# Performance work log

Hardware: AMD Instinct MI355X
Metric: run time of the kernel (lower is better)

## Reference

```python
import jax, jax.numpy as jnp
import numpy as np

N_HEAD = 16
ROPE_THETA = 10000.0


def setup_inputs() -> dict:
    key = jax.random.key(0)
    k0, k1, k2 = jax.random.split(key, 3)
    B, T, C = 2, 2048, 1024
    s = 0.02  # GPT-2 style init scale
    return {
        "x": jax.random.normal(k0, (B, T, C), jnp.float32),
        "w_attn": jax.random.normal(k1, (C, 3 * C), jnp.float32) * s,
        "b_attn": jnp.zeros((3 * C,), jnp.float32),
        "w_proj": jax.random.normal(k2, (C, C), jnp.float32) * s,
        "b_proj": jnp.zeros((C,), jnp.float32),
    }


def _rope(x):
    # x: [B, H, T, D]; interleaved-pair rotary (lucidrains rotate_queries_or_keys)
    T, D = x.shape[-2], x.shape[-1]
    inv_freq = 1.0 / (ROPE_THETA ** (jnp.arange(0, D, 2, dtype=jnp.float32) / D))
    freqs = jnp.arange(T, dtype=jnp.float32)[:, None] * inv_freq[None, :]  # [T, D/2]
    emb = jnp.repeat(freqs, 2, axis=-1)  # [T, D], each freq duplicated per pair
    cos, sin = jnp.cos(emb), jnp.sin(emb)
    xr = x.reshape(*x.shape[:-1], D // 2, 2)
    x1, x2 = xr[..., 0], xr[..., 1]
    rot = jnp.stack((-x2, x1), axis=-1).reshape(x.shape)  # rotate_half
    return x * cos + rot * sin


def reference(x, w_attn, b_attn, w_proj, b_proj):
    B, T, C = x.shape
    H = N_HEAD
    D = C // H
    qkv = x @ w_attn + b_attn                      # [B, T, 3C]
    q, k, v = jnp.split(qkv, 3, axis=-1)

    def heads(t):
        return t.reshape(B, T, H, D).transpose(0, 2, 1, 3)  # [B, H, T, D]

    q, k, v = heads(q), heads(k), heads(v)
    q = _rope(q)
    k = _rope(k)

    att = jnp.einsum("bhqd,bhkd->bhqk", q, k) * (1.0 / np.sqrt(D))
    causal = jnp.tril(jnp.ones((T, T), dtype=bool))
    att = jnp.where(causal, att, -jnp.inf)
    att = jax.nn.softmax(att, axis=-1)
    y = jnp.einsum("bhqk,bhkd->bhqd", att, v)
    y = y.transpose(0, 2, 1, 3).reshape(B, T, C)
    return y @ w_proj + b_proj
```

## Files before the change

### kernel.cpp

```cpp
#include <hip/hip_runtime.h>
#include <hip/hip_bf16.h>
#include <stdint.h>

typedef __hip_bfloat16 bf16;
typedef __attribute__((ext_vector_type(8))) short bf16x8;
typedef __attribute__((ext_vector_type(4))) short bf16x4;
typedef __attribute__((ext_vector_type(4))) float f32x4;

__device__ inline float bf2f(bf16 v) { return __bfloat162float(v); }
__device__ inline bf16 f2bf(float f) { return __float2bfloat16(f); }

__device__ inline void glds16(const void* g, void* l) {
    __builtin_amdgcn_global_load_lds(
        (const __attribute__((address_space(1))) uint32_t*)g,
        (__attribute__((address_space(3))) uint32_t*)l, 16, 0, 0);
}

__device__ inline void conv_wt_tile(const float* __restrict__ W,
                                    bf16* __restrict__ Wt, int N, int K,
                                    int bx, int by, int tid, bf16 (*t)[72])
{
    const int n0 = bx * 64, k0 = by * 64;
#pragma unroll
    for (int p = 0; p < 4; ++p) {
        int idx = p * 256 + tid;
        int kr = idx >> 4, c4 = idx & 15;
        float4 f = *(const float4*)(W + (size_t)(k0 + kr) * N + n0 + c4 * 4);
        t[kr][c4 * 4 + 0] = f2bf(f.x); t[kr][c4 * 4 + 1] = f2bf(f.y);
        t[kr][c4 * 4 + 2] = f2bf(f.z); t[kr][c4 * 4 + 3] = f2bf(f.w);
    }
    __syncthreads();
#pragma unroll
    for (int p = 0; p < 2; ++p) {
        int idx = p * 256 + tid;
        int nr = idx >> 3, ch = idx & 7;
        union { bf16x8 v; bf16 e[8]; } u;
#pragma unroll
        for (int j = 0; j < 8; ++j) u.e[j] = t[ch * 8 + j][nr];
        *(bf16x8*)(Wt + (size_t)(n0 + nr) * K + k0 + ch * 8) = u.v;
    }
}

__global__ __launch_bounds__(256) void prep(
    const float* __restrict__ x, bf16* __restrict__ xbf,
    const float* __restrict__ w_attn, bf16* __restrict__ wat,
    const float* __restrict__ w_proj, bf16* __restrict__ wpt,
    float2* __restrict__ tab)
{
    __shared__ bf16 t[64][72];
    const int bid = blockIdx.x;
    const int tid = threadIdx.x;
    if (bid < 2048) {
        size_t i = ((size_t)bid * 256 + tid) * 8;
        float4 f0 = *(const float4*)(x + i);
        float4 f1 = *(const float4*)(x + i + 4);
        union { bf16x8 v; bf16 e[8]; } u;
        u.e[0] = f2bf(f0.x); u.e[1] = f2bf(f0.y); u.e[2] = f2bf(f0.z); u.e[3] = f2bf(f0.w);
        u.e[4] = f2bf(f1.x); u.e[5] = f2bf(f1.y); u.e[6] = f2bf(f1.z); u.e[7] = f2bf(f1.w);
        *(bf16x8*)(xbf + i) = u.v;
    } else if (bid < 2816) {
        int idx = bid - 2048;
        conv_wt_tile(w_attn, wat, 3072, 1024, idx % 48, idx / 48, tid, t);
    } else if (bid < 3072) {
        int idx = bid - 2816;
        conv_wt_tile(w_proj, wpt, 1024, 1024, idx % 16, idx / 16, tid, t);
    } else {
        int gid = (bid - 3072) * 256 + tid;
        int p = gid & 31, tt = gid >> 5;
        float invf = expf(-(float)(2 * p) * (9.210340371976184f / 64.0f));
        float sn, cs;
        sincosf((float)tt * invf, &sn, &cs);
        tab[gid] = make_float2(cs, sn);
    }
}

__global__ __launch_bounds__(256) void gemm_qkv(
    const bf16* __restrict__ A, const bf16* __restrict__ Bt,
    const float* __restrict__ bias, const float2* __restrict__ tab,
    bf16* __restrict__ qh, bf16* __restrict__ kh, bf16* __restrict__ vt)
{
    const int K = 1024;
    __shared__ __align__(16) bf16 sa[128 * 64];
    __shared__ __align__(16) bf16 sb[128 * 64];

    const int tid  = threadIdx.x;
    const int wave = tid >> 6, lane = tid & 63;
    const int quad = lane >> 4, l16 = lane & 15;
    const int wm = wave >> 1, wn = wave & 1;
    const int row0 = blockIdx.x * 128, n0 = blockIdx.y * 128;

    f32x4 acc[4][4] = {};

    const int srow = lane >> 3;
    const int schk = lane & 7;

    for (int k0 = 0; k0 < K; k0 += 64) {
        __syncthreads();
#pragma unroll
        for (int half = 0; half < 2; ++half) {
#pragma unroll
            for (int g = 0; g < 2; ++g) {
                int rowb = half * 64 + wave * 16 + g * 8;
                int row  = rowb + srow;
                glds16(A + (size_t)(row0 + row) * K + k0 + ((schk ^ row) & 7) * 8,
                       &sa[rowb * 64]);
                glds16(Bt + (size_t)(n0 + row) * K + k0 + ((schk ^ row) & 7) * 8,
                       &sb[rowb * 64]);
            }
        }
        __syncthreads();

#pragma unroll
        for (int kk = 0; kk < 2; ++kk) {
            bf16x8 af[4], bfr[4];
#pragma unroll
            for (int mi = 0; mi < 4; ++mi) {
                int row = wm * 64 + mi * 16 + l16;
                af[mi] = *(const bf16x8*)&sa[row * 64 + (((kk * 4 + quad) ^ row) & 7) * 8];
            }
#pragma unroll
            for (int ni = 0; ni < 4; ++ni) {
                int row = wn * 64 + ni * 16 + l16;
                bfr[ni] = *(const bf16x8*)&sb[row * 64 + (((kk * 4 + quad) ^ row) & 7) * 8];
            }
#pragma unroll
            for (int mi = 0; mi < 4; ++mi)
#pragma unroll
                for (int ni = 0; ni < 4; ++ni)
                    acc[mi][ni] = __builtin_amdgcn_mfma_f32_16x16x32_bf16(
                        af[mi], bfr[ni], acc[mi][ni], 0, 0, 0);
        }
    }

    const float QS = 0.125f * 1.44269504088896f;
#pragma unroll
    for (int ni = 0; ni < 4; ++ni) {
        int col = n0 + wn * 64 + ni * 16 + l16;
        float bvv = bias[col];
        int sec = col >> 10;
        int cd  = col & 1023;
        int h   = cd >> 6, d = cd & 63;
        if (sec == 2) {
#pragma unroll
            for (int mi = 0; mi < 4; ++mi) {
                int trow = row0 + wm * 64 + mi * 16 + quad * 4;
                int tt0 = trow & 2047, bb = trow >> 11;
                union { bf16x4 v; bf16 e[4]; } pv;
#pragma unroll
                for (int r = 0; r < 4; ++r) pv.e[r] = f2bf(acc[mi][ni][r] + bvv);
                *(bf16x4*)(vt + ((size_t)((bb * 16 + h) * 64 + d)) * 2048 + tt0) = pv.v;
            }
        } else {
            int p   = d >> 1;
            bool odd = (d & 1) != 0;
#pragma unroll
            for (int mi = 0; mi < 4; ++mi) {
#pragma unroll
                for (int r = 0; r < 4; ++r) {
                    int row = row0 + wm * 64 + mi * 16 + quad * 4 + r;
                    float v = acc[mi][ni][r] + bvv;
                    float vp = __shfl_xor(v, 1);
                    int tt = row & 2047, b = row >> 11;
                    float2 cssn = tab[tt * 32 + p];
                    float ro = odd ? (v * cssn.x + vp * cssn.y)
                                   : (v * cssn.x - vp * cssn.y);
                    size_t dst = (((size_t)(b * 16 + h)) * 2048 + tt) * 64 + d;
                    if (sec == 0) qh[dst] = f2bf(ro * QS);
                    else          kh[dst] = f2bf(ro);
                }
            }
        }
    }
}

__global__ __launch_bounds__(256) void gemm_proj(
    const bf16* __restrict__ A, const bf16* __restrict__ Bt,
    const float* __restrict__ bias, float* __restrict__ out)
{
    const int N = 1024, K = 1024;
    __shared__ __align__(16) bf16 sa[64 * 64];
    __shared__ __align__(16) bf16 sb[128 * 64];

    const int tid  = threadIdx.x;
    const int wave = tid >> 6, lane = tid & 63;
    const int quad = lane >> 4, l16 = lane & 15;
    const int row0 = blockIdx.x * 64, n0 = blockIdx.y * 128;

    f32x4 acc[4][2] = {};

    const int srow = lane >> 3;
    const int schk = lane & 7;

    for (int k0 = 0; k0 < K; k0 += 64) {
        __syncthreads();
#pragma unroll
        for (int g = 0; g < 2; ++g) {
            int rowb = wave * 16 + g * 8;
            int row  = rowb + srow;
            glds16(A + (size_t)(row0 + row) * K + k0 + ((schk ^ row) & 7) * 8,
                   &sa[rowb * 64]);
        }
#pragma unroll
        for (int g = 0; g < 4; ++g) {
            int rowb = wave * 32 + g * 8;
            int row  = rowb + srow;
            glds16(Bt + (size_t)(n0 + row) * K + k0 + ((schk ^ row) & 7) * 8,
                   &sb[rowb * 64]);
        }
        __syncthreads();

#pragma unroll
        for (int kk = 0; kk < 2; ++kk) {
            bf16x8 af[4], bfr[2];
#pragma unroll
            for (int mi = 0; mi < 4; ++mi) {
                int row = mi * 16 + l16;
                af[mi] = *(const bf16x8*)&sa[row * 64 + (((kk * 4 + quad) ^ row) & 7) * 8];
            }
#pragma unroll
            for (int ni = 0; ni < 2; ++ni) {
                int row = wave * 32 + ni * 16 + l16;
                bfr[ni] = *(const bf16x8*)&sb[row * 64 + (((kk * 4 + quad) ^ row) & 7) * 8];
            }
#pragma unroll
            for (int mi = 0; mi < 4; ++mi)
#pragma unroll
                for (int ni = 0; ni < 2; ++ni)
                    acc[mi][ni] = __builtin_amdgcn_mfma_f32_16x16x32_bf16(
                        af[mi], bfr[ni], acc[mi][ni], 0, 0, 0);
        }
    }

#pragma unroll
    for (int ni = 0; ni < 2; ++ni) {
        int col = n0 + wave * 32 + ni * 16 + l16;
        float bvv = bias[col];
#pragma unroll
        for (int mi = 0; mi < 4; ++mi) {
#pragma unroll
            for (int r = 0; r < 4; ++r) {
                int row = row0 + mi * 16 + quad * 4 + r;
                out[(size_t)row * N + col] = acc[mi][ni][r] + bvv;
            }
        }
    }
}

__global__ __launch_bounds__(256) void attn_k(
    const bf16* __restrict__ qg, const bf16* __restrict__ kg,
    const bf16* __restrict__ vtg, bf16* __restrict__ y)
{
    __shared__ __align__(16) bf16 sK[128 * 64];
    __shared__ __align__(16) bf16 sV[64 * 128];
    __shared__ __align__(16) bf16 pL[4][16][136];

    const int tid  = threadIdx.x;
    const int wave = tid >> 6, lane = tid & 63;
    const int quad = lane >> 4, l16 = lane & 15;
    const int bh   = blockIdx.x;
    const int qt   = 31 - (int)blockIdx.y;
    const bf16* Q  = qg  + (size_t)bh * 2048 * 64;
    const bf16* K  = kg  + (size_t)bh * 2048 * 64;
    const bf16* Vt = vtg + (size_t)bh * 64 * 2048;
    const int b = bh >> 4, h = bh & 15;

    const int q0 = qt * 64 + wave * 16;

    bf16x8 aq[2];
    aq[0] = *(const bf16x8*)(Q + (size_t)(q0 + l16) * 64 + quad * 8);
    aq[1] = *(const bf16x8*)(Q + (size_t)(q0 + l16) * 64 + 32 + quad * 8);

    union { bf16x8 v; short e[8]; } uo;
#pragma unroll
    for (int j = 0; j < 8; ++j) uo.e[j] = (short)0x3F80;
    const bf16x8 vones = uo.v;

    f32x4 o[4] = {};
    f32x4 ls   = {};
    float m_r[4] = {-1e30f, -1e30f, -1e30f, -1e30f};
    const float THR = 8.0f;

    for (int kt = 0; kt <= q0 + 15; kt += 128) {
        __syncthreads();
#pragma unroll
        for (int c = 0; c < 4; ++c) {
            int key = wave * 32 + c * 8 + (lane >> 3);
            int p = lane & 7;
            glds16(K + (size_t)(kt + key) * 64 + ((p ^ key) & 7) * 8,
                   &sK[(wave * 32 + c * 8) * 64]);
        }
#pragma unroll
        for (int c = 0; c < 4; ++c) {
            int d = wave * 16 + c * 4 + (lane >> 4);
            int p = lane & 15;
            glds16(Vt + (size_t)d * 2048 + kt + ((p ^ d) & 15) * 8,
                   &sV[(wave * 16 + c * 4) * 128]);
        }
        __syncthreads();

        const int nlast = min(7, (q0 - kt) >> 4);
        f32x4 sc[8];
        __builtin_amdgcn_s_setprio(1);
#pragma unroll
        for (int nt = 0; nt < 8; ++nt) {
            if (nt > nlast) continue;
            int key = nt * 16 + l16;
            f32x4 s0 = {};
            bf16x8 bk0 = *(const bf16x8*)&sK[key * 64 + ((quad ^ key) & 7) * 8];
            s0 = __builtin_amdgcn_mfma_f32_16x16x32_bf16(aq[0], bk0, s0, 0, 0, 0);
            bf16x8 bk1 = *(const bf16x8*)&sK[key * 64 + (((4 + quad) ^ key) & 7) * 8];
            sc[nt] = __builtin_amdgcn_mfma_f32_16x16x32_bf16(aq[1], bk1, s0, 0, 0, 0);
        }
        __builtin_amdgcn_s_setprio(0);
        {
            const int diag = (q0 - kt) >> 4;
            if (diag <= 7) {
                int key = kt + diag * 16 + l16;
#pragma unroll
                for (int r = 0; r < 4; ++r) {
                    int row = q0 + quad * 4 + r;
                    if (key > row) sc[diag][r] = -1e30f;
                }
            }
        }
        float rowmax[4] = {-1e30f, -1e30f, -1e30f, -1e30f};
#pragma unroll
        for (int nt = 0; nt < 8; ++nt) {
            if (nt > nlast) continue;
#pragma unroll
            for (int r = 0; r < 4; ++r) rowmax[r] = fmaxf(rowmax[r], sc[nt][r]);
        }
        bool okl = (rowmax[0] <= m_r[0] + THR) && (rowmax[1] <= m_r[1] + THR) &&
                   (rowmax[2] <= m_r[2] + THR) && (rowmax[3] <= m_r[3] + THR);
        if (!__all((int)okl)) {
#pragma unroll
            for (int off = 1; off < 16; off <<= 1)
#pragma unroll
                for (int r = 0; r < 4; ++r)
                    rowmax[r] = fmaxf(rowmax[r], __shfl_xor(rowmax[r], off));
            float alpha[4];
#pragma unroll
            for (int r = 0; r < 4; ++r) {
                float mn = fmaxf(m_r[r], rowmax[r]);
                alpha[r] = exp2f(m_r[r] - mn);
                m_r[r] = mn;
            }
#pragma unroll
            for (int nt = 0; nt < 4; ++nt)
#pragma unroll
                for (int r = 0; r < 4; ++r) o[nt][r] *= alpha[r];
#pragma unroll
            for (int r = 0; r < 4; ++r) ls[r] *= alpha[r];
        }
#pragma unroll
        for (int nt = 0; nt < 8; ++nt) {
            if (nt > nlast) continue;
#pragma unroll
            for (int r = 0; r < 4; ++r) sc[nt][r] = exp2f(sc[nt][r] - m_r[r]);
        }

#pragma unroll
        for (int nt = 0; nt < 8; ++nt) {
            if (nt > nlast) continue;
            int blk = (2 * nt + (l16 >> 3)) ^ quad;
#pragma unroll
            for (int r = 0; r < 4; ++r)
                pL[wave][quad * 4 + r][blk * 8 + (l16 & 7)] = f2bf(sc[nt][r]);
        }
        if (nlast < 7 && !(nlast & 1)) {
            int blk = (2 * (nlast + 1) + (l16 >> 3)) ^ quad;
#pragma unroll
            for (int r = 0; r < 4; ++r)
                pL[wave][quad * 4 + r][blk * 8 + (l16 & 7)] = f2bf(0.f);
        }
        __builtin_amdgcn_s_setprio(1);
#pragma unroll
        for (int c = 0; c < 4; ++c) {
            if (c > (nlast >> 1)) continue;
            bf16x8 pa = *(const bf16x8*)&pL[wave][l16][(((4 * c + quad) ^ (l16 >> 2)) * 8)];
            ls = __builtin_amdgcn_mfma_f32_16x16x32_bf16(pa, vones, ls, 0, 0, 0);
#pragma unroll
            for (int dnt = 0; dnt < 4; ++dnt) {
                int d = dnt * 16 + l16;
                int cc = c * 4 + quad;
                bf16x8 vb = *(const bf16x8*)&sV[d * 128 + ((cc ^ d) & 15) * 8];
                o[dnt] = __builtin_amdgcn_mfma_f32_16x16x32_bf16(pa, vb, o[dnt], 0, 0, 0);
            }
        }
        __builtin_amdgcn_s_setprio(0);
    }

#pragma unroll
    for (int r = 0; r < 4; ++r) {
        float inv = 1.0f / ls[r];
        int qq = q0 + quad * 4 + r;
#pragma unroll
        for (int nt = 0; nt < 4; ++nt) {
            int d = nt * 16 + l16;
            y[((size_t)(b * 2048 + qq)) * 1024 + h * 64 + d] = f2bf(o[nt][r] * inv);
        }
    }
}

extern "C" void kernel_launch(void* const* d_in, const int* in_sizes, int n_in,
                              void* d_out, int out_size, void* d_ws, size_t ws_size,
                              hipStream_t stream) {
    const float* x      = (const float*)d_in[0];
    const float* w_attn = (const float*)d_in[1];
    const float* b_attn = (const float*)d_in[2];
    const float* w_proj = (const float*)d_in[3];
    const float* b_proj = (const float*)d_in[4];
    float* out = (float*)d_out;

    bf16* xbf = (bf16*)d_ws;
    bf16* wat = xbf + (size_t)4194304;
    bf16* wpt = wat + (size_t)3145728;
    float2* tab = (float2*)(wpt + (size_t)1048576);
    bf16* qh  = wpt + (size_t)1048576 + 262144;
    bf16* kh  = qh  + (size_t)4194304;
    bf16* vt  = kh  + (size_t)4194304;
    bf16* yws = vt  + (size_t)4194304;

    dim3 blk(256);
    prep<<<dim3(3328), blk, 0, stream>>>(x, xbf, w_attn, wat, w_proj, wpt, tab);
    gemm_qkv<<<dim3(32, 24), blk, 0, stream>>>(xbf, wat, b_attn, tab, qh, kh, vt);
    attn_k<<<dim3(32, 32), blk, 0, stream>>>(qh, kh, vt, yws);
    gemm_proj<<<dim3(64, 8), blk, 0, stream>>>(yws, wpt, b_proj, out);
    (void)in_sizes; (void)n_in; (void)ws_size; (void)out_size;
}
```

Measured before the change: 210.4 us.

## Compute transposed QK^T scores and move P to the PV operand via shuffles, dropping the LDS staging

Swaps the MFMA operands for QK^T so each lane holds scores for a single query row, which turns the row max into one scalar per lane reduced with two cross-quad shuffles instead of per-register butterfly reductions. The softmax probabilities are packed to bf16 in registers and redistributed into the A-operand layout of the PV MFMA using lane shuffles, removing the per-wave LDS buffer and its stores and loads. This trades LDS traffic and shared memory for extra ds_bpermute shuffles and select instructions, and the rescale factors must now be broadcast back to the output layout with shuffles.

```diff
diff --git a/kernel.cpp b/kernel.cpp
--- a/kernel.cpp
+++ b/kernel.cpp
@@ -14,6 +14,12 @@
     __builtin_amdgcn_global_load_lds(
         (const __attribute__((address_space(1))) uint32_t*)g,
         (__attribute__((address_space(3))) uint32_t*)l, 16, 0, 0);
+}
+
+__device__ inline uint32_t packbf(float a, float b) {
+    union { bf16 e[2]; uint32_t u; } v;
+    v.e[0] = f2bf(a); v.e[1] = f2bf(b);
+    return v.u;
 }
 
 __device__ inline void conv_wt_tile(const float* __restrict__ W,
@@ -252,7 +258,6 @@
 {
     __shared__ __align__(16) bf16 sK[128 * 64];
     __shared__ __align__(16) bf16 sV[64 * 128];
-    __shared__ __align__(16) bf16 pL[4][16][136];
 
     const int tid  = threadIdx.x;
     const int wave = tid >> 6, lane = tid & 63;
@@ -277,7 +282,7 @@
 
     f32x4 o[4] = {};
     f32x4 ls   = {};
-    float m_r[4] = {-1e30f, -1e30f, -1e30f, -1e30f};
+    float m_r  = -1e30f;
     const float THR = 8.0f;
 
     for (int kt = 0; kt <= q0 + 15; kt += 128) {
@@ -307,84 +312,81 @@
             int key = nt * 16 + l16;
             f32x4 s0 = {};
             bf16x8 bk0 = *(const bf16x8*)&sK[key * 64 + ((quad ^ key) & 7) * 8];
-            s0 = __builtin_amdgcn_mfma_f32_16x16x32_bf16(aq[0], bk0, s0, 0, 0, 0);
+            s0 = __builtin_amdgcn_mfma_f32_16x16x32_bf16(bk0, aq[0], s0, 0, 0, 0);
             bf16x8 bk1 = *(const bf16x8*)&sK[key * 64 + (((4 + quad) ^ key) & 7) * 8];
-            sc[nt] = __builtin_amdgcn_mfma_f32_16x16x32_bf16(aq[1], bk1, s0, 0, 0, 0);
+            sc[nt] = __builtin_amdgcn_mfma_f32_16x16x32_bf16(bk1, aq[1], s0, 0, 0, 0);
         }
         __builtin_amdgcn_s_setprio(0);
         {
             const int diag = (q0 - kt) >> 4;
             if (diag <= 7) {
-                int key = kt + diag * 16 + l16;
-#pragma unroll
-                for (int r = 0; r < 4; ++r) {
-                    int row = q0 + quad * 4 + r;
-                    if (key > row) sc[diag][r] = -1e30f;
-                }
-            }
-        }
-        float rowmax[4] = {-1e30f, -1e30f, -1e30f, -1e30f};
+                int keyg = kt + diag * 16 + quad * 4;
+                int row  = q0 + l16;
+#pragma unroll
+                for (int r = 0; r < 4; ++r)
+                    if (keyg + r > row) sc[diag][r] = -1e30f;
+            }
+        }
+        float mloc = -1e30f;
 #pragma unroll
         for (int nt = 0; nt < 8; ++nt) {
             if (nt > nlast) continue;
 #pragma unroll
-            for (int r = 0; r < 4; ++r) rowmax[r] = fmaxf(rowmax[r], sc[nt][r]);
-        }
-        bool okl = (rowmax[0] <= m_r[0] + THR) && (rowmax[1] <= m_r[1] + THR) &&
-                   (rowmax[2] <= m_r[2] + THR) && (rowmax[3] <= m_r[3] + THR);
+            for (int r = 0; r < 4; ++r) mloc = fmaxf(mloc, sc[nt][r]);
+        }
+        bool okl = (mloc <= m_r + THR);
         if (!__all((int)okl)) {
-#pragma unroll
-            for (int off = 1; off < 16; off <<= 1)
-#pragma unroll
-                for (int r = 0; r < 4; ++r)
-                    rowmax[r] = fmaxf(rowmax[r], __shfl_xor(rowmax[r], off));
-            float alpha[4];
-#pragma unroll
-            for (int r = 0; r < 4; ++r) {
-                float mn = fmaxf(m_r[r], rowmax[r]);
-                alpha[r] = exp2f(m_r[r] - mn);
-                m_r[r] = mn;
-            }
+            float mf = mloc;
+            mf = fmaxf(mf, __shfl_xor(mf, 16));
+            mf = fmaxf(mf, __shfl_xor(mf, 32));
+            float mn = fmaxf(m_r, mf);
+            float alpha = exp2f(m_r - mn);
+            m_r = mn;
+            float a4[4];
+#pragma unroll
+            for (int r = 0; r < 4; ++r)
+                a4[r] = __shfl(alpha, (quad << 4) + quad * 4 + r);
 #pragma unroll
             for (int nt = 0; nt < 4; ++nt)
 #pragma unroll
-                for (int r = 0; r < 4; ++r) o[nt][r] *= alpha[r];
-#pragma unroll
-            for (int r = 0; r < 4; ++r) ls[r] *= alpha[r];
-        }
+                for (int r = 0; r < 4; ++r) o[nt][r] *= a4[r];
+#pragma unroll
+            for (int r = 0; r < 4; ++r) ls[r] *= a4[r];
+        }
+        uint32_t pk[8][2];
 #pragma unroll
         for (int nt = 0; nt < 8; ++nt) {
-            if (nt > nlast) continue;
-#pragma unroll
-            for (int r = 0; r < 4; ++r) sc[nt][r] = exp2f(sc[nt][r] - m_r[r]);
-        }
-
-#pragma unroll
-        for (int nt = 0; nt < 8; ++nt) {
-            if (nt > nlast) continue;
-            int blk = (2 * nt + (l16 >> 3)) ^ quad;
-#pragma unroll
-            for (int r = 0; r < 4; ++r)
-                pL[wave][quad * 4 + r][blk * 8 + (l16 & 7)] = f2bf(sc[nt][r]);
-        }
-        if (nlast < 7 && !(nlast & 1)) {
-            int blk = (2 * (nlast + 1) + (l16 >> 3)) ^ quad;
-#pragma unroll
-            for (int r = 0; r < 4; ++r)
-                pL[wave][quad * 4 + r][blk * 8 + (l16 & 7)] = f2bf(0.f);
+            if (nt <= nlast) {
+                float p0 = exp2f(sc[nt][0] - m_r), p1 = exp2f(sc[nt][1] - m_r);
+                float p2 = exp2f(sc[nt][2] - m_r), p3 = exp2f(sc[nt][3] - m_r);
+                pk[nt][0] = packbf(p0, p1);
+                pk[nt][1] = packbf(p2, p3);
+            } else { pk[nt][0] = 0u; pk[nt][1] = 0u; }
         }
         __builtin_amdgcn_s_setprio(1);
+        const int s0l = ((quad & 1) << 5) + l16;
 #pragma unroll
         for (int c = 0; c < 4; ++c) {
             if (c > (nlast >> 1)) continue;
-            bf16x8 pa = *(const bf16x8*)&pL[wave][l16][(((4 * c + quad) ^ (l16 >> 2)) * 8)];
-            ls = __builtin_amdgcn_mfma_f32_16x16x32_bf16(pa, vones, ls, 0, 0, 0);
+            uint32_t a0 = (uint32_t)__shfl((int)pk[2 * c][0], s0l);
+            uint32_t a1 = (uint32_t)__shfl((int)pk[2 * c][1], s0l);
+            uint32_t a2 = (uint32_t)__shfl((int)pk[2 * c][0], s0l + 16);
+            uint32_t a3 = (uint32_t)__shfl((int)pk[2 * c][1], s0l + 16);
+            uint32_t b0 = (uint32_t)__shfl((int)pk[2 * c + 1][0], s0l);
+            uint32_t b1 = (uint32_t)__shfl((int)pk[2 * c + 1][1], s0l);
+            uint32_t b2 = (uint32_t)__shfl((int)pk[2 * c + 1][0], s0l + 16);
+            uint32_t b3 = (uint32_t)__shfl((int)pk[2 * c + 1][1], s0l + 16);
+            union { bf16x8 v; uint32_t d[4]; } pa;
+            bool hi = quad >= 2;
+            pa.d[0] = hi ? b0 : a0; pa.d[1] = hi ? b1 : a1;
+            pa.d[2] = hi ? b2 : a2; pa.d[3] = hi ? b3 : a3;
+            ls = __builtin_amdgcn_mfma_f32_16x16x32_bf16(pa.v, vones, ls, 0, 0, 0);
 #pragma unroll
             for (int dnt = 0; dnt < 4; ++dnt) {
                 int d = dnt * 16 + l16;
                 int cc = c * 4 + quad;
                 bf16x8 vb = *(const bf16x8*)&sV[d * 128 + ((cc ^ d) & 15) * 8];
-                o[dnt] = __builtin_amdgcn_mfma_f32_16x16x32_bf16(pa, vb, o[dnt], 0, 0, 0);
+                o[dnt] = __builtin_amdgcn_mfma_f32_16x16x32_bf16(pa.v, vb, o[dnt], 0, 0, 0);
             }
         }
         __builtin_amdgcn_s_setprio(0);
```

Measured after the change: 214.8 us. +2.1%, slower.
